# Kernel optimization log

Measured on AMD Instinct MI355X. Metric: run time of the kernel, lower is better.

Reference implementation:

```python
import jax, jax.numpy as jnp
import numpy as np

B, S, D, H, E, K = 4, 1024, 1024, 4096, 8, 2


def setup_inputs() -> dict:
    key = jax.random.key(0)
    k1, k2, k3, k4 = jax.random.split(key, 4)
    x = jax.random.normal(k1, (B, S, D), dtype=jnp.float32)
    # expert params: two-layer MLP per expert, stacked along expert axis
    W1 = jax.random.normal(k2, (E, D, H), dtype=jnp.float32) * 0.02
    b1 = jnp.zeros((E, H), dtype=jnp.float32)
    W2 = jax.random.normal(k3, (E, H, D), dtype=jnp.float32) * 0.02
    b2 = jnp.zeros((E, D), dtype=jnp.float32)
    # hash-router assignments: k expert ids per token (stands in for HashRouter output)
    assign = jax.random.randint(k4, (B, S, K), 0, E, dtype=jnp.int64)
    return {"x": x, "W1": W1, "b1": b1, "W2": W2, "b2": b2, "assign": assign, "k": K}


def reference(x, W1, b1, W2, b2, assign, k):
    E_ = W1.shape[0]
    # mask[b,s,e] = 1 if expert e appears in assign[b,s,:] (matches (assign==idx).any(-1),
    # so a duplicated assignment contributes once, exactly like the torch loop)
    mask = (assign[..., None] == jnp.arange(E_)[None, None, None, :]).any(axis=-2)
    # run every token through every expert, then mask-combine (dense MoE reference)
    h = jax.nn.relu(jnp.einsum('bsd,edh->bseh', x, W1) + b1)      # [B,S,E,H]
    y = jnp.einsum('bseh,ehd->bsed', h, W2) + b2                  # [B,S,E,D]
    out = jnp.einsum('bsed,bse->bsd', y, mask.astype(x.dtype))
    return out / k
```

## Files before the change

kernel.cpp:

```cpp
#include <hip/hip_runtime.h>
#include <hip/hip_bf16.h>

#define DIM_D 1024
#define DIM_H 4096
#define NUM_E 8
#define NUM_TOK 4096
#define MAXROWS 8320

typedef __attribute__((ext_vector_type(8))) short short8;
typedef __attribute__((ext_vector_type(4))) float floatx4;

__device__ __forceinline__ unsigned short f2bf(float f) {
  union { float f; unsigned int u; } v; v.f = f;
  unsigned int r = v.u + 0x7fffu + ((v.u >> 16) & 1u);
  return (unsigned short)(r >> 16);
}

__device__ __forceinline__ void async_copy16(const void* g, void* l) {
  __builtin_amdgcn_global_load_lds(
      (__attribute__((address_space(1))) unsigned int*)(g),
      (__attribute__((address_space(3))) unsigned int*)(l), 16, 0, 0);
}


__global__ void route_scan(const int* __restrict__ assign, int* __restrict__ counts,
                           int* __restrict__ offsets, int* __restrict__ cursors) {
  __shared__ int hist[NUM_E];
  int tid = threadIdx.x;
  if (tid < NUM_E) hist[tid] = 0;
  __syncthreads();
  for (int t = tid; t < NUM_TOK; t += 256) {
    int e0 = assign[2 * t], e1 = assign[2 * t + 1];
    atomicAdd(&hist[e0], 1);
    if (e1 != e0) atomicAdd(&hist[e1], 1);
  }
  __syncthreads();
  if (tid == 0) {
    int acc = 0;
    for (int e = 0; e < NUM_E; e++) {
      counts[e] = hist[e]; offsets[e] = acc; cursors[e] = acc; acc += hist[e];
    }
  }
}

__global__ void gather_k(const float* __restrict__ x, const int* __restrict__ assign,
                         int* __restrict__ cursors, int* __restrict__ tok2row,
                         unsigned short* __restrict__ Xg) {
  int t = blockIdx.x;
  __shared__ int sr[2];
  if (threadIdx.x == 0) {
    int e0 = assign[2 * t], e1 = assign[2 * t + 1];
    int r0 = atomicAdd(&cursors[e0], 1);
    int r1 = (e1 != e0) ? atomicAdd(&cursors[e1], 1) : -1;
    tok2row[2 * t] = r0; tok2row[2 * t + 1] = r1;
    sr[0] = r0; sr[1] = r1;
  }
  __syncthreads();
  int r0 = sr[0], r1 = sr[1];
  const float4* xv = (const float4*)(x + (size_t)t * DIM_D);
  float4 v0 = xv[threadIdx.x * 2];
  float4 v1 = xv[threadIdx.x * 2 + 1];
  unsigned short h[8];
  h[0] = f2bf(v0.x); h[1] = f2bf(v0.y); h[2] = f2bf(v0.z); h[3] = f2bf(v0.w);
  h[4] = f2bf(v1.x); h[5] = f2bf(v1.y); h[6] = f2bf(v1.z); h[7] = f2bf(v1.w);
  uint4 pack = *(uint4*)h;
  *(uint4*)(Xg + (size_t)r0 * DIM_D + threadIdx.x * 8) = pack;
  if (r1 >= 0)
    *(uint4*)(Xg + (size_t)r1 * DIM_D + threadIdx.x * 8) = pack;
}

__global__ __launch_bounds__(256) void transpose_cvt2(
    const float* __restrict__ W1, const float* __restrict__ W2,
    unsigned short* __restrict__ W1t, unsigned short* __restrict__ W2t) {
  __shared__ float tile[128][33];
  const int z = blockIdx.y;
  const int e = z >> 1, which = z & 1;
  const int R = which ? DIM_H : DIM_D;
  const int C = which ? DIM_D : DIM_H;
  const int nbx = C / 32;
  const int bx = blockIdx.x % nbx;
  const int by = blockIdx.x / nbx;
  const float* ip = (which ? W2 : W1) + (size_t)e * R * C;
  unsigned short* op = (which ? W2t : W1t) + (size_t)e * R * C;
  const int tid = threadIdx.x;

  int rr = tid >> 3;
  int c4 = (tid & 7) * 4;
#pragma unroll
  for (int p = 0; p < 4; p++) {
    int r = p * 32 + rr;
    float4 v = *(const float4*)(ip + (size_t)(by * 128 + r) * C + bx * 32 + c4);
    tile[r][c4 + 0] = v.x; tile[r][c4 + 1] = v.y;
    tile[r][c4 + 2] = v.z; tile[r][c4 + 3] = v.w;
  }
  __syncthreads();
  int cc = tid >> 4;
  int r8 = (tid & 15) * 8;
#pragma unroll
  for (int q = 0; q < 2; q++) {
    int c = q * 16 + cc;
    unsigned short h[8];
#pragma unroll
    for (int j = 0; j < 8; j++) h[j] = f2bf(tile[r8 + j][c]);
    *(uint4*)(op + (size_t)(bx * 32 + c) * R + by * 128 + r8) = *(const uint4*)h;
  }
}

template <int MODE, int KTOT>
__global__ __launch_bounds__(256) void moe_gemm(
    const unsigned short* __restrict__ Ain, const unsigned short* __restrict__ Bt,
    const float* __restrict__ bias, const int* __restrict__ counts,
    const int* __restrict__ offsets,
    unsigned short* __restrict__ Hout, float* __restrict__ Yout,
    int lda, int ldb, int N) {
  int e, half;
  if (MODE == 0) { e = blockIdx.z; half = 0; }
  else           { e = blockIdx.z >> 1; half = blockIdx.z & 1; }
  const int cnt = counts[e];
  int mt_, nt_;
  if (MODE == 0) {
    nt_ = (blockIdx.x & 7) | ((blockIdx.y & 3) << 3);
    mt_ = (blockIdx.x >> 3) | ((blockIdx.y >> 2) << 2);
  } else {
    nt_ = blockIdx.x; mt_ = blockIdx.y;
  }
  const int m0 = mt_ * 128;
  if (m0 >= cnt) return;
  const int n0 = nt_ * 128;
  const int rowbase = offsets[e];
  const unsigned short* A = Ain + (size_t)half * KTOT;

  __shared__ unsigned short sh[2 * 128 * 64];
  unsigned short* As = sh;
  unsigned short* Bs = sh + 128 * 64;

  const int tid = threadIdx.x;
  const int w = tid >> 6;
  const int lane = tid & 63;
  const int l15 = lane & 15, l4 = lane >> 4;
  const int wm = w >> 1, wn = w & 1;
  const int lrow = lane >> 3, lslot = lane & 7;
  const int lchunk = lslot ^ lrow;

  const unsigned short* gA[4]; const unsigned short* gB[4];
  void* dA[4]; void* dB[4];
  const unsigned short* Bbase = Bt + (size_t)e * N * ldb + (size_t)half * KTOT;
#pragma unroll
  for (int p = 0; p < 4; p++) {
    int rw = p * 32 + w * 8;
    gA[p] = A + (size_t)(rowbase + m0 + rw + lrow) * lda + lchunk * 8;
    gB[p] = Bbase + (size_t)(n0 + rw + lrow) * ldb + lchunk * 8;
    dA[p] = (char*)As + rw * 128;
    dB[p] = (char*)Bs + rw * 128;
  }

  floatx4 acc[4][4];
#pragma unroll
  for (int i = 0; i < 4; i++)
#pragma unroll
    for (int j = 0; j < 4; j++) acc[i][j] = (floatx4){0.f, 0.f, 0.f, 0.f};

  int arow[4], brow[4], sl[2];
  sl[0] = ((l4 + 0) ^ (l15 & 7)) * 8;
  sl[1] = ((l4 + 4) ^ (l15 & 7)) * 8;
#pragma unroll
  for (int mt = 0; mt < 4; mt++) arow[mt] = (wm * 64 + mt * 16 + l15) * 64;
#pragma unroll
  for (int nt = 0; nt < 4; nt++) brow[nt] = (wn * 64 + nt * 16 + l15) * 64;

  for (int k0 = 0; k0 < KTOT; k0 += 64) {
    __syncthreads();
#pragma unroll
    for (int p = 0; p < 4; p++) async_copy16(gA[p], dA[p]);
#pragma unroll
    for (int p = 0; p < 4; p++) async_copy16(gB[p], dB[p]);
#pragma unroll
    for (int p = 0; p < 4; p++) { gA[p] += 64; gB[p] += 64; }
    __syncthreads();
#pragma unroll
    for (int s = 0; s < 2; s++) {
      short8 a[4], b[4];
#pragma unroll
      for (int mt = 0; mt < 4; mt++) a[mt] = *(const short8*)(As + arow[mt] + sl[s]);
#pragma unroll
      for (int nt = 0; nt < 4; nt++) b[nt] = *(const short8*)(Bs + brow[nt] + sl[s]);
#pragma unroll
      for (int mt = 0; mt < 4; mt++)
#pragma unroll
        for (int nt = 0; nt < 4; nt++)
          acc[mt][nt] = __builtin_amdgcn_mfma_f32_16x16x32_bf16(a[mt], b[nt], acc[mt][nt], 0, 0, 0);
    }
  }

  __syncthreads();
  float* sbuf = (float*)sh + w * 1088;
  const bool addb = (MODE == 0) || (half == 0);
  const float* be = bias + (size_t)e * N + n0 + wn * 64;
  float* yplane = (MODE == 1) ? (Yout + (size_t)half * MAXROWS * N) : nullptr;
#pragma unroll
  for (int mt = 0; mt < 4; mt++) {
#pragma unroll
    for (int nt = 0; nt < 4; nt++) {
      float bv = addb ? be[nt * 16 + l15] : 0.f;
#pragma unroll
      for (int r = 0; r < 4; r++) {
        float v = acc[mt][nt][r] + bv;
        if (MODE == 0) v = fmaxf(v, 0.f);
        sbuf[(l4 * 4 + r) * 68 + nt * 16 + l15] = v;
      }
    }
    __asm__ __volatile__("s_waitcnt lgkmcnt(0)" ::: "memory");
#pragma unroll
    for (int pass = 0; pass < 4; pass++) {
      int row = pass * 4 + l4;
      int col4 = l15 * 4;
      int gm = m0 + wm * 64 + mt * 16 + row;
      float4 v = *(const float4*)&sbuf[row * 68 + col4];
      if (gm < cnt) {
        size_t off = (size_t)(rowbase + gm) * N + n0 + wn * 64 + col4;
        if (MODE == 0) {
          ushort4 h;
          h.x = f2bf(v.x); h.y = f2bf(v.y); h.z = f2bf(v.z); h.w = f2bf(v.w);
          *(ushort4*)(Hout + off) = h;
        } else {
          *(float4*)(yplane + off) = v;
        }
      }
    }
    __asm__ __volatile__("s_waitcnt lgkmcnt(0)" ::: "memory");
  }
}

__global__ void combine_k(const float* __restrict__ Yg, const int* __restrict__ tok2row,
                          const int* __restrict__ kptr, float* __restrict__ out) {
  int t = blockIdx.x;
  int r0 = tok2row[2 * t], r1 = tok2row[2 * t + 1];
  float invk = 1.0f / (float)kptr[0];
  int d = threadIdx.x * 4;
  const size_t plane = (size_t)MAXROWS * DIM_D;
  float4 v = *(const float4*)(Yg + (size_t)r0 * DIM_D + d);
  float4 u = *(const float4*)(Yg + plane + (size_t)r0 * DIM_D + d);
  v.x += u.x; v.y += u.y; v.z += u.z; v.w += u.w;
  if (r1 >= 0) {
    float4 a = *(const float4*)(Yg + (size_t)r1 * DIM_D + d);
    float4 b = *(const float4*)(Yg + plane + (size_t)r1 * DIM_D + d);
    v.x += a.x + b.x; v.y += a.y + b.y; v.z += a.z + b.z; v.w += a.w + b.w;
  }
  float4 o; o.x = v.x * invk; o.y = v.y * invk; o.z = v.z * invk; o.w = v.w * invk;
  *(float4*)(out + (size_t)t * DIM_D + d) = o;
}


extern "C" void kernel_launch(void* const* d_in, const int* in_sizes, int n_in,
                              void* d_out, int out_size, void* d_ws, size_t ws_size,
                              hipStream_t stream) {
  const float* x = (const float*)d_in[0];
  const float* W1 = (const float*)d_in[1];
  const float* b1 = (const float*)d_in[2];
  const float* W2 = (const float*)d_in[3];
  const float* b2 = (const float*)d_in[4];
  const int* assign = (const int*)d_in[5];
  const int* kptr = (const int*)d_in[6];
  float* out = (float*)d_out;

  char* p = (char*)d_ws;
  int* counts = (int*)p; p += 256;
  int* offsets = (int*)p; p += 256;
  int* cursors = (int*)p; p += 256;
  int* tok2row = (int*)p; p += NUM_TOK * 2 * 4;
  unsigned short* W1t = (unsigned short*)p; p += (size_t)NUM_E * DIM_D * DIM_H * 2;
  unsigned short* Xg = (unsigned short*)p; p += (size_t)MAXROWS * DIM_D * 2;
  unsigned short* Hg = (unsigned short*)p; p += (size_t)MAXROWS * DIM_H * 2;
  unsigned short* W2t = (unsigned short*)p; p += (size_t)NUM_E * DIM_D * DIM_H * 2;
  float* Yg = (float*)W1t;

  route_scan<<<1, 256, 0, stream>>>(assign, counts, offsets, cursors);
  gather_k<<<NUM_TOK, 128, 0, stream>>>(x, assign, cursors, tok2row, Xg);

  transpose_cvt2<<<dim3(1024, 16), 256, 0, stream>>>(W1, W2, W1t, W2t);

  moe_gemm<0, DIM_D><<<dim3(32, 32, NUM_E), 256, 0, stream>>>(
      Xg, W1t, b1, counts, offsets, Hg, nullptr, DIM_D, DIM_D, DIM_H);
  moe_gemm<1, DIM_H / 2><<<dim3(8, 32, NUM_E * 2), 256, 0, stream>>>(
      Hg, W2t, b2, counts, offsets, nullptr, Yg, DIM_H, DIM_H, DIM_D);

  combine_k<<<NUM_TOK, 256, 0, stream>>>(Yg, tok2row, kptr, out);
}
```

Baseline: 634.2 us.

## Compute token row slots in a deterministic scan and use 64x64 swizzled transpose tiles

Routing now builds per-thread histograms, prefix-scans them and writes tok2row directly, so the gather kernel no longer needs global atomics or a single-thread setup step per token. Row order becomes deterministic. Separately, the weight transpose/convert kernel switches from 128x32 padded tiles to 64x64 tiles with an XOR swizzle, using float4 LDS stores and avoiding bank conflicts on the transposed reads. The single-block routing scan stays serial over 256 entries per expert, which may add a little latency.

```diff
diff --git a/kernel.cpp b/kernel.cpp
--- a/kernel.cpp
+++ b/kernel.cpp
@@ -22,41 +22,54 @@
       (__attribute__((address_space(3))) unsigned int*)(l), 16, 0, 0);
 }
 
-
-__global__ void route_scan(const int* __restrict__ assign, int* __restrict__ counts,
-                           int* __restrict__ offsets, int* __restrict__ cursors) {
-  __shared__ int hist[NUM_E];
-  int tid = threadIdx.x;
-  if (tid < NUM_E) hist[tid] = 0;
-  __syncthreads();
-  for (int t = tid; t < NUM_TOK; t += 256) {
-    int e0 = assign[2 * t], e1 = assign[2 * t + 1];
-    atomicAdd(&hist[e0], 1);
-    if (e1 != e0) atomicAdd(&hist[e1], 1);
+__global__ __launch_bounds__(256) void route_scan(
+    const int* __restrict__ assign, int* __restrict__ counts,
+    int* __restrict__ offsets, int* __restrict__ tok2row) {
+  __shared__ int hist[256][NUM_E];
+  __shared__ int base[NUM_E];
+  const int tid = threadIdx.x;
+  const int t0 = tid * 16;
+#pragma unroll
+  for (int e = 0; e < NUM_E; e++) hist[tid][e] = 0;
+  const int4* ap = (const int4*)(assign + t0 * 2);
+  for (int i = 0; i < 8; i++) {
+    int4 v = ap[i];
+    hist[tid][v.x]++; if (v.y != v.x) hist[tid][v.y]++;
+    hist[tid][v.z]++; if (v.w != v.z) hist[tid][v.w]++;
+  }
+  __syncthreads();
+  if (tid < NUM_E) {
+    int acc = 0;
+    for (int i = 0; i < 256; i++) { int v = hist[i][tid]; hist[i][tid] = acc; acc += v; }
+    base[tid] = acc;
   }
   __syncthreads();
   if (tid == 0) {
     int acc = 0;
     for (int e = 0; e < NUM_E; e++) {
-      counts[e] = hist[e]; offsets[e] = acc; cursors[e] = acc; acc += hist[e];
-    }
-  }
-}
-
-__global__ void gather_k(const float* __restrict__ x, const int* __restrict__ assign,
-                         int* __restrict__ cursors, int* __restrict__ tok2row,
+      int tot = base[e];
+      counts[e] = tot; offsets[e] = acc; base[e] = acc; acc += tot;
+    }
+  }
+  __syncthreads();
+#pragma unroll
+  for (int e = 0; e < NUM_E; e++) hist[tid][e] += base[e];
+  for (int i = 0; i < 8; i++) {
+    int4 v = ap[i];
+    int t = t0 + 2 * i;
+    int4 o;
+    o.x = hist[tid][v.x]++;
+    o.y = (v.y != v.x) ? hist[tid][v.y]++ : -1;
+    o.z = hist[tid][v.z]++;
+    o.w = (v.w != v.z) ? hist[tid][v.w]++ : -1;
+    *(int4*)(tok2row + 2 * t) = o;
+  }
+}
+
+__global__ void gather_x(const float* __restrict__ x, const int* __restrict__ tok2row,
                          unsigned short* __restrict__ Xg) {
   int t = blockIdx.x;
-  __shared__ int sr[2];
-  if (threadIdx.x == 0) {
-    int e0 = assign[2 * t], e1 = assign[2 * t + 1];
-    int r0 = atomicAdd(&cursors[e0], 1);
-    int r1 = (e1 != e0) ? atomicAdd(&cursors[e1], 1) : -1;
-    tok2row[2 * t] = r0; tok2row[2 * t + 1] = r1;
-    sr[0] = r0; sr[1] = r1;
-  }
-  __syncthreads();
-  int r0 = sr[0], r1 = sr[1];
+  int r0 = tok2row[2 * t], r1 = tok2row[2 * t + 1];
   const float4* xv = (const float4*)(x + (size_t)t * DIM_D);
   float4 v0 = xv[threadIdx.x * 2];
   float4 v1 = xv[threadIdx.x * 2 + 1];
@@ -69,40 +82,48 @@
     *(uint4*)(Xg + (size_t)r1 * DIM_D + threadIdx.x * 8) = pack;
 }
 
-__global__ __launch_bounds__(256) void transpose_cvt2(
+__global__ __launch_bounds__(256) void transpose_cvt64(
     const float* __restrict__ W1, const float* __restrict__ W2,
     unsigned short* __restrict__ W1t, unsigned short* __restrict__ W2t) {
-  __shared__ float tile[128][33];
+  __shared__ float tile[64 * 64];
   const int z = blockIdx.y;
   const int e = z >> 1, which = z & 1;
   const int R = which ? DIM_H : DIM_D;
   const int C = which ? DIM_D : DIM_H;
-  const int nbx = C / 32;
+  const int nbx = C / 64;
   const int bx = blockIdx.x % nbx;
   const int by = blockIdx.x / nbx;
-  const float* ip = (which ? W2 : W1) + (size_t)e * R * C;
-  unsigned short* op = (which ? W2t : W1t) + (size_t)e * R * C;
+  const float* ip = (which ? W2 : W1) + (size_t)e * R * C + (size_t)(by * 64) * C + bx * 64;
+  unsigned short* op = (which ? W2t : W1t) + (size_t)e * R * C + (size_t)(bx * 64) * R + by * 64;
   const int tid = threadIdx.x;
 
-  int rr = tid >> 3;
-  int c4 = (tid & 7) * 4;
-#pragma unroll
-  for (int p = 0; p < 4; p++) {
-    int r = p * 32 + rr;
-    float4 v = *(const float4*)(ip + (size_t)(by * 128 + r) * C + bx * 32 + c4);
-    tile[r][c4 + 0] = v.x; tile[r][c4 + 1] = v.y;
-    tile[r][c4 + 2] = v.z; tile[r][c4 + 3] = v.w;
-  }
-  __syncthreads();
-  int cc = tid >> 4;
-  int r8 = (tid & 15) * 8;
-#pragma unroll
-  for (int q = 0; q < 2; q++) {
-    int c = q * 16 + cc;
-    unsigned short h[8];
-#pragma unroll
-    for (int j = 0; j < 8; j++) h[j] = f2bf(tile[r8 + j][c]);
-    *(uint4*)(op + (size_t)(bx * 32 + c) * R + by * 128 + r8) = *(const uint4*)h;
+  {
+    int chunk = tid & 15;
+    int rb = tid >> 4;
+#pragma unroll
+    for (int p = 0; p < 4; p++) {
+      int r = rb + p * 16;
+      float4 v = *(const float4*)(ip + (size_t)r * C + chunk * 4);
+      int sc = chunk ^ rb;
+      *(float4*)&tile[r * 64 + sc * 4] = v;
+    }
+  }
+  __syncthreads();
+  {
+    int c = tid & 63;
+    int rb = (tid >> 6) * 8;
+    int ch = c >> 2, cl = c & 3;
+#pragma unroll
+    for (int q = 0; q < 2; q++) {
+      int r0 = rb + q * 32;
+      unsigned short h[8];
+#pragma unroll
+      for (int j = 0; j < 8; j++) {
+        int r = r0 + j;
+        h[j] = f2bf(tile[r * 64 + ((ch ^ (r & 15)) * 4) + cl]);
+      }
+      *(uint4*)(op + (size_t)c * R + r0) = *(const uint4*)h;
+    }
   }
 }
 
@@ -266,7 +287,6 @@
   char* p = (char*)d_ws;
   int* counts = (int*)p; p += 256;
   int* offsets = (int*)p; p += 256;
-  int* cursors = (int*)p; p += 256;
   int* tok2row = (int*)p; p += NUM_TOK * 2 * 4;
   unsigned short* W1t = (unsigned short*)p; p += (size_t)NUM_E * DIM_D * DIM_H * 2;
   unsigned short* Xg = (unsigned short*)p; p += (size_t)MAXROWS * DIM_D * 2;
@@ -274,10 +294,10 @@
   unsigned short* W2t = (unsigned short*)p; p += (size_t)NUM_E * DIM_D * DIM_H * 2;
   float* Yg = (float*)W1t;
 
-  route_scan<<<1, 256, 0, stream>>>(assign, counts, offsets, cursors);
-  gather_k<<<NUM_TOK, 128, 0, stream>>>(x, assign, cursors, tok2row, Xg);
-
-  transpose_cvt2<<<dim3(1024, 16), 256, 0, stream>>>(W1, W2, W1t, W2t);
+  route_scan<<<1, 256, 0, stream>>>(assign, counts, offsets, tok2row);
+  gather_x<<<NUM_TOK, 128, 0, stream>>>(x, tok2row, Xg);
+
+  transpose_cvt64<<<dim3(1024, 16), 256, 0, stream>>>(W1, W2, W1t, W2t);
 
   moe_gemm<0, DIM_D><<<dim3(32, 32, NUM_E), 256, 0, stream>>>(
       Xg, W1t, b1, counts, offsets, Hg, nullptr, DIM_D, DIM_D, DIM_H);
```

New measurement: 556.7 us. -12.2%, faster.
